# Kernel optimization log

Measured on AMD Instinct MI355X. Metric: run time of the kernel, lower is better.

## Reference

```python
import jax, jax.numpy as jnp
import numpy as np

B, L, D, H, T = 64, 512, 768, 384, 9  # batch, seq_len, hidden, hidden//2, num_tags


def setup_inputs() -> dict:
    key = jax.random.key(0)
    ks = jax.random.split(key, 8)
    return {
        "encoder_out": jax.random.normal(ks[0], (B, L, D), jnp.float32),
        "ner_labels": jax.random.randint(ks[1], (B, L), 0, T),
        "mask": jnp.ones((B, L), jnp.bool_),
        "W1": jax.random.normal(ks[2], (D, H), jnp.float32) / np.sqrt(D).astype(np.float32),
        "b1": jnp.zeros((H,), jnp.float32),
        "W2": jax.random.normal(ks[3], (H, T), jnp.float32) / np.sqrt(H).astype(np.float32),
        "b2": jnp.zeros((T,), jnp.float32),
        "start_trans": jax.random.uniform(ks[4], (T,), jnp.float32, -0.1, 0.1),
        "end_trans": jax.random.uniform(ks[5], (T,), jnp.float32, -0.1, 0.1),
        "trans": jax.random.uniform(ks[6], (T, T), jnp.float32, -0.1, 0.1),
    }


def _crf_nll(emissions, tags, mask, start_trans, end_trans, trans):
    """-mean log-likelihood, matching pytorch-crf forward (reduction='mean')."""
    maskf = mask.astype(emissions.dtype)
    # ---- numerator: score of the gold tag path ----
    emit = jnp.take_along_axis(emissions, tags[..., None], axis=-1)[..., 0]  # [B,L]
    emit_score = jnp.sum(emit * maskf, axis=1)
    tr = trans[tags[:, :-1], tags[:, 1:]]  # [B,L-1]
    tr_score = jnp.sum(tr * maskf[:, 1:], axis=1)
    last_idx = jnp.sum(mask.astype(jnp.int32), axis=1) - 1
    last_tags = jnp.take_along_axis(tags, last_idx[:, None], axis=1)[:, 0]
    numer = start_trans[tags[:, 0]] + emit_score + tr_score + end_trans[last_tags]
    # ---- denominator: forward algorithm (log partition) via scan ----
    alpha0 = start_trans[None, :] + emissions[:, 0]          # [B,T]
    em_rest = jnp.swapaxes(emissions[:, 1:], 0, 1)           # [L-1,B,T]
    mk_rest = jnp.swapaxes(maskf[:, 1:], 0, 1)               # [L-1,B]

    def step(alpha, xs):
        e_t, m_t = xs
        nxt = jax.nn.logsumexp(alpha[:, :, None] + trans[None, :, :] + e_t[:, None, :], axis=1)
        return jnp.where(m_t[:, None] > 0, nxt, alpha), None

    alpha, _ = jax.lax.scan(step, alpha0, (em_rest, mk_rest))
    denom = jax.nn.logsumexp(alpha + end_trans[None, :], axis=1)
    return -jnp.mean(numer - denom)


def reference(encoder_out, ner_labels, mask, W1, b1, W2, b2, start_trans, end_trans, trans):
    # proj: Linear -> GELU (exact erf, torch default) -> Dropout (identity in eval)
    h = jax.nn.gelu(encoder_out @ W1 + b1, approximate=False)
    emissions = h @ W2 + b2  # [B,L,T]
    return _crf_nll(emissions, ner_labels, mask, start_trans, end_trans, trans)
```

## Files before the change

kernel.cpp:

```cpp
#include <hip/hip_runtime.h>
#include <hip/hip_bf16.h>
#include <math.h>

#define B_ 64
#define L_ 512
#define D_ 768
#define H_ 384
#define T_ 9
#define M_ (B_ * L_)

typedef __attribute__((ext_vector_type(8))) short short8;
typedef __attribute__((ext_vector_type(4))) float f32x4;

__device__ __forceinline__ float gelu_exact(float x) {
    return 0.5f * x * (1.0f + erff(x * 0.70710678118654752440f));
}

__device__ __forceinline__ unsigned short f2bf(float f) {
    unsigned u = __float_as_uint(f);
    u += 0x7FFFu + ((u >> 16) & 1u);
    return (unsigned short)(u >> 16);
}

__device__ __forceinline__ float wredf(float v) {
#pragma unroll
    for (int m = 32; m >= 1; m >>= 1) v += __shfl_xor(v, m, 64);
    return v;
}

__global__ __launch_bounds__(256) void prep_kernel(
    const float* __restrict__ W1, const float* __restrict__ W2,
    unsigned short* __restrict__ W1F, unsigned short* __restrict__ W2F)
{
    const int g    = blockIdx.x * 4 + (threadIdx.x >> 6);
    const int lane = threadIdx.x & 63;
    const int lm   = lane & 15;
    const int q    = lane >> 4;
    if (g < 576) {
        const int nt = g / 24;
        const int kc = g - nt * 24;
        const int n  = nt * 16 + lm;
        short8 v;
#pragma unroll
        for (int j = 0; j < 8; ++j)
            v[j] = (short)f2bf(W1[(size_t)(kc * 32 + q * 8 + j) * H_ + n]);
        *(short8*)(W1F + ((size_t)g * 64 + lane) * 8) = v;
    } else if (g < 588) {
        const int kk = g - 576;
        short8 v;
#pragma unroll
        for (int j = 0; j < 8; ++j) {
            int k = kk * 32 + q * 8 + j;
            v[j] = (lm < 9) ? (short)f2bf(W2[(size_t)k * T_ + lm]) : (short)0;
        }
        *(short8*)(W2F + ((size_t)kk * 64 + lane) * 8) = v;
    }
}

__global__ __launch_bounds__(256, 2) void emis_mfma_kernel(
    const float* __restrict__ X,
    const unsigned short* __restrict__ W1F,
    const float* __restrict__ b1,
    const unsigned short* __restrict__ W2F,
    const float* __restrict__ b2,
    float* __restrict__ em)
{
    __shared__ unsigned short Hs[64 * 392];
    unsigned short* As = Hs;

    const int t    = threadIdx.x;
    const int lane = t & 63;
    const int w    = t >> 6;
    const int lm   = lane & 15;
    const int q    = lane >> 4;
    const int row0 = blockIdx.x * 64;

    const int ar  = t >> 2;
    const int ako = (t & 3) << 3;
    const float* xp = X + (size_t)(row0 + ar) * D_ + ako;

    f32x4 acc[4][6];
#pragma unroll
    for (int mt = 0; mt < 4; ++mt)
#pragma unroll
        for (int i = 0; i < 6; ++i) acc[mt][i] = (f32x4)0.f;

    float4 x0 = *(const float4*)(xp);
    float4 x1 = *(const float4*)(xp + 4);
    short8 bcur[6];
#pragma unroll
    for (int i = 0; i < 6; ++i)
        bcur[i] = *(const short8*)(W1F + (((size_t)(w * 6 + i) * 24) * 64 + lane) * 8);
    {
        short8 v;
        v[0] = (short)f2bf(x0.x); v[1] = (short)f2bf(x0.y);
        v[2] = (short)f2bf(x0.z); v[3] = (short)f2bf(x0.w);
        v[4] = (short)f2bf(x1.x); v[5] = (short)f2bf(x1.y);
        v[6] = (short)f2bf(x1.z); v[7] = (short)f2bf(x1.w);
        *(short8*)&As[ar * 40 + ako] = v;
    }

    int buf = 0;
    for (int kc = 0; kc < 24; ++kc) {
        const bool notlast = (kc < 23);
        float4 xn0, xn1;
        short8 bnxt[6];
        if (notlast) {
            xn0 = *(const float4*)(xp + (kc + 1) * 32);
            xn1 = *(const float4*)(xp + (kc + 1) * 32 + 4);
#pragma unroll
            for (int i = 0; i < 6; ++i)
                bnxt[i] = *(const short8*)(W1F +
                    (((size_t)(w * 6 + i) * 24 + kc + 1) * 64 + lane) * 8);
        }
        __syncthreads();
        short8 af[4];
#pragma unroll
        for (int mt = 0; mt < 4; ++mt)
            af[mt] = *(const short8*)&As[buf * 2560 + (mt * 16 + lm) * 40 + (q << 3)];
#pragma unroll
        for (int mt = 0; mt < 4; ++mt)
#pragma unroll
            for (int i = 0; i < 6; ++i)
                acc[mt][i] = __builtin_amdgcn_mfma_f32_16x16x32_bf16(
                    af[mt], bcur[i], acc[mt][i], 0, 0, 0);
        if (notlast) {
            short8 v;
            v[0] = (short)f2bf(xn0.x); v[1] = (short)f2bf(xn0.y);
            v[2] = (short)f2bf(xn0.z); v[3] = (short)f2bf(xn0.w);
            v[4] = (short)f2bf(xn1.x); v[5] = (short)f2bf(xn1.y);
            v[6] = (short)f2bf(xn1.z); v[7] = (short)f2bf(xn1.w);
            *(short8*)&As[(buf ^ 1) * 2560 + ar * 40 + ako] = v;
#pragma unroll
            for (int i = 0; i < 6; ++i) bcur[i] = bnxt[i];
            buf ^= 1;
        }
    }
    __syncthreads();

#pragma unroll
    for (int i = 0; i < 6; ++i) {
        const int col = w * 96 + i * 16 + lm;
        const float b1v = b1[col];
#pragma unroll
        for (int mt = 0; mt < 4; ++mt)
#pragma unroll
            for (int r = 0; r < 4; ++r) {
                float h = gelu_exact(acc[mt][i][r] + b1v);
                Hs[(mt * 16 + q * 4 + r) * 392 + col] = f2bf(h);
            }
    }
    __syncthreads();

    f32x4 e = (f32x4)0.f;
#pragma unroll
    for (int kk = 0; kk < 12; ++kk) {
        short8 ah = *(const short8*)&Hs[(w * 16 + lm) * 392 + kk * 32 + (q << 3)];
        short8 bw = *(const short8*)(W2F + ((size_t)(kk * 64 + lane)) * 8);
        e = __builtin_amdgcn_mfma_f32_16x16x32_bf16(ah, bw, e, 0, 0, 0);
    }
    if (lm < 9) {
        const float b2v = b2[lm];
#pragma unroll
        for (int r = 0; r < 4; ++r)
            em[(size_t)(row0 + w * 16 + q * 4 + r) * T_ + lm] = e[r] + b2v;
    }
}

__global__ __launch_bounds__(576) void crf_kernel(
    const float* __restrict__ em,
    const int* __restrict__ labels,
    const unsigned char* __restrict__ maskb,
    const float* __restrict__ st,
    const float* __restrict__ et,
    const float* __restrict__ tr,
    float* __restrict__ outb)
{
    const int b = blockIdx.x;
    const int t = threadIdx.x;

    __shared__ float es[64 * 73];
    __shared__ float Ms[64 * 81];
    __shared__ float trs[81];
    __shared__ float trsT[81];
    __shared__ float red[2];
    __shared__ unsigned char msh[L_];
    __shared__ int lbs[L_];

    const int mstride =
        (maskb[0] != 0 && maskb[1] == 0 && maskb[2] == 0 && maskb[3] == 0) ? 4 : 1;

    const float* eb = em + (size_t)b * L_ * T_;
    for (int i = t; i < L_ * T_; i += 576) {
        int tt = i / T_, j = i - tt * T_;
        es[(tt >> 3) * 73 + (tt & 7) * 9 + j] = eb[i];
    }
    if (t < 81) {
        float v = tr[t];
        trs[t] = v;
        int k = t / 9, j = t - k * 9;
        trsT[j * 9 + k] = v;
    }
    for (int i = t; i < L_; i += 576) {
        msh[i] = maskb[((size_t)b * L_ + i) * (size_t)mstride];
        lbs[i] = labels[b * L_ + i];
    }
    __syncthreads();

    {
        const int c  = t / 9;
        const int i0 = t - c * 9;
        float V[9];
#pragma unroll
        for (int j = 0; j < 9; ++j) V[j] = (j == i0) ? 0.f : -1e30f;

        const int sbeg = (c == 0) ? 1 : 0;
        for (int s = sbeg; s < 8; ++s) {
            int tt = c * 8 + s;
            if (msh[tt]) {
                const float* ep = &es[c * 73 + s * 9];
                float nv[9];
#pragma unroll
                for (int j = 0; j < 9; ++j) {
                    const float* trc = &trsT[j * 9];
                    float a[9];
#pragma unroll
                    for (int k = 0; k < 9; ++k) a[k] = V[k] + trc[k];
                    float mx = a[0];
#pragma unroll
                    for (int k = 1; k < 9; ++k) mx = fmaxf(mx, a[k]);
                    float sum = 0.f;
#pragma unroll
                    for (int k = 0; k < 9; ++k) sum += __expf(a[k] - mx);
                    nv[j] = ep[j] + mx + __logf(sum);
                }
#pragma unroll
                for (int j = 0; j < 9; ++j) V[j] = nv[j];
            }
        }
#pragma unroll
        for (int j = 0; j < 9; ++j) Ms[c * 81 + i0 * 9 + j] = V[j];
    }
    __syncthreads();

    const int lane = t & 63;
    const int w    = t >> 6;
    if (w == 0) {
        const int jj = lane < 9 ? lane : 8;
        float alpha = (lane < 9) ? st[jj] + es[jj] : -1e30f;
        for (int c = 0; c < 64; ++c) {
            float a[9];
#pragma unroll
            for (int i = 0; i < 9; ++i) {
                float av = __shfl(alpha, i, 64);
                a[i] = av + Ms[c * 81 + i * 9 + jj];
            }
            float mx = a[0];
#pragma unroll
            for (int i = 1; i < 9; ++i) mx = fmaxf(mx, a[i]);
            float sum = 0.f;
#pragma unroll
            for (int i = 0; i < 9; ++i) sum += __expf(a[i] - mx);
            float nv = mx + __logf(sum);
            if (lane < 9) alpha = nv;
        }
        float v = (lane < 9) ? alpha + et[jj] : -1e30f;
        float mx = v;
#pragma unroll
        for (int m = 32; m >= 1; m >>= 1) mx = fmaxf(mx, __shfl_xor(mx, m, 64));
        float s = __expf(v - mx);
        s = wredf(s);
        if (lane == 0) red[0] = mx + __logf(s);
    } else if (w == 1) {
        float emit_s = 0.f, tr_sc = 0.f, mcnt = 0.f;
        for (int tt = lane; tt < L_; tt += 64) {
            if (msh[tt]) {
                mcnt += 1.f;
                int tag = lbs[tt];
                emit_s += es[(tt >> 3) * 73 + (tt & 7) * 9 + tag];
                if (tt >= 1) tr_sc += trs[lbs[tt - 1] * 9 + tag];
            }
        }
        emit_s = wredf(emit_s);
        tr_sc  = wredf(tr_sc);
        mcnt   = wredf(mcnt);
        if (lane == 0) {
            int last = (int)mcnt - 1;
            red[1] = st[lbs[0]] + emit_s + tr_sc + et[lbs[last]];
        }
    }
    __syncthreads();
    if (t == 0) outb[b] = red[1] - red[0];
}

__global__ __launch_bounds__(64) void finalize_kernel(
    const float* __restrict__ bv, float* __restrict__ out)
{
    float v = bv[threadIdx.x];
    v = wredf(v);
    if (threadIdx.x == 0) out[0] = -v * (1.0f / (float)B_);
}

extern "C" void kernel_launch(void* const* d_in, const int* in_sizes, int n_in,
                              void* d_out, int out_size, void* d_ws, size_t ws_size,
                              hipStream_t stream) {
    const float*         enc    = (const float*)d_in[0];
    const int*           labels = (const int*)d_in[1];
    const unsigned char* mask   = (const unsigned char*)d_in[2];
    const float*         W1     = (const float*)d_in[3];
    const float*         b1     = (const float*)d_in[4];
    const float*         W2     = (const float*)d_in[5];
    const float*         b2     = (const float*)d_in[6];
    const float*         st     = (const float*)d_in[7];
    const float*         et     = (const float*)d_in[8];
    const float*         tr     = (const float*)d_in[9];

    float* em           = (float*)d_ws;
    float* bvals        = em + (size_t)M_ * T_;
    unsigned short* W1F = (unsigned short*)(bvals + B_);
    unsigned short* W2F = W1F + (size_t)576 * 64 * 8;

    prep_kernel<<<147, 256, 0, stream>>>(W1, W2, W1F, W2F);
    emis_mfma_kernel<<<M_ / 64, 256, 0, stream>>>(enc, W1F, b1, W2F, b2, em);
    crf_kernel<<<B_, 576, 0, stream>>>(em, labels, mask, st, et, tr, bvals);
    finalize_kernel<<<1, 64, 0, stream>>>(bvals, (float*)d_out);
}
```

Baseline: 237.3 us.

## Deepen GEMM prefetch, halve CRF chunks, fold finalize into atomic add

The emission GEMM loop is fully unrolled with a two-stage register prefetch of both X and W1 fragments, and uses a lightweight barrier (waitcnt lgkmcnt plus s_barrier) in place of __syncthreads so outstanding global loads need not drain. The CRF kernel now uses 32 chunks of 16 steps with 288 threads, caching the transition matrix in registers. The finalize kernel is removed: the output is zeroed in the prep kernel and each CRF block atomically adds its share. This trades a longer serial chunk scan and more register pressure for fewer launches and better latency hiding, and the atomic sum makes the result order nondeterministic.

```diff
diff --git a/kernel.cpp b/kernel.cpp
--- a/kernel.cpp
+++ b/kernel.cpp
@@ -28,10 +28,16 @@
     return v;
 }
 
+__device__ __forceinline__ void sync_lds() {
+    asm volatile("s_waitcnt lgkmcnt(0)\n\ts_barrier" ::: "memory");
+}
+
 __global__ __launch_bounds__(256) void prep_kernel(
     const float* __restrict__ W1, const float* __restrict__ W2,
-    unsigned short* __restrict__ W1F, unsigned short* __restrict__ W2F)
+    unsigned short* __restrict__ W1F, unsigned short* __restrict__ W2F,
+    float* __restrict__ out)
 {
+    if (blockIdx.x == 0 && threadIdx.x == 0) out[0] = 0.f;
     const int g    = blockIdx.x * 4 + (threadIdx.x >> 6);
     const int lane = threadIdx.x & 63;
     const int lm   = lane & 15;
@@ -85,55 +91,58 @@
 #pragma unroll
         for (int i = 0; i < 6; ++i) acc[mt][i] = (f32x4)0.f;
 
-    float4 x0 = *(const float4*)(xp);
-    float4 x1 = *(const float4*)(xp + 4);
-    short8 bcur[6];
-#pragma unroll
-    for (int i = 0; i < 6; ++i)
-        bcur[i] = *(const short8*)(W1F + (((size_t)(w * 6 + i) * 24) * 64 + lane) * 8);
     {
+        float4 p0 = *(const float4*)(xp);
+        float4 p1 = *(const float4*)(xp + 4);
         short8 v;
-        v[0] = (short)f2bf(x0.x); v[1] = (short)f2bf(x0.y);
-        v[2] = (short)f2bf(x0.z); v[3] = (short)f2bf(x0.w);
-        v[4] = (short)f2bf(x1.x); v[5] = (short)f2bf(x1.y);
-        v[6] = (short)f2bf(x1.z); v[7] = (short)f2bf(x1.w);
+        v[0] = (short)f2bf(p0.x); v[1] = (short)f2bf(p0.y);
+        v[2] = (short)f2bf(p0.z); v[3] = (short)f2bf(p0.w);
+        v[4] = (short)f2bf(p1.x); v[5] = (short)f2bf(p1.y);
+        v[6] = (short)f2bf(p1.z); v[7] = (short)f2bf(p1.w);
         *(short8*)&As[ar * 40 + ako] = v;
     }
-
-    int buf = 0;
+    float4 xv[2][2];
+    xv[0][0] = *(const float4*)(xp + 32);  xv[0][1] = *(const float4*)(xp + 36);
+    xv[1][0] = *(const float4*)(xp + 64);  xv[1][1] = *(const float4*)(xp + 68);
+    short8 bb[2][6];
+#pragma unroll
+    for (int i = 0; i < 6; ++i) {
+        bb[0][i] = *(const short8*)(W1F + (((size_t)(w * 6 + i) * 24 + 0) * 64 + lane) * 8);
+        bb[1][i] = *(const short8*)(W1F + (((size_t)(w * 6 + i) * 24 + 1) * 64 + lane) * 8);
+    }
+
+#pragma unroll
     for (int kc = 0; kc < 24; ++kc) {
-        const bool notlast = (kc < 23);
-        float4 xn0, xn1;
-        short8 bnxt[6];
-        if (notlast) {
-            xn0 = *(const float4*)(xp + (kc + 1) * 32);
-            xn1 = *(const float4*)(xp + (kc + 1) * 32 + 4);
-#pragma unroll
-            for (int i = 0; i < 6; ++i)
-                bnxt[i] = *(const short8*)(W1F +
-                    (((size_t)(w * 6 + i) * 24 + kc + 1) * 64 + lane) * 8);
-        }
-        __syncthreads();
+        const int s = kc & 1;
+        sync_lds();
         short8 af[4];
 #pragma unroll
         for (int mt = 0; mt < 4; ++mt)
-            af[mt] = *(const short8*)&As[buf * 2560 + (mt * 16 + lm) * 40 + (q << 3)];
+            af[mt] = *(const short8*)&As[s * 2560 + (mt * 16 + lm) * 40 + (q << 3)];
 #pragma unroll
         for (int mt = 0; mt < 4; ++mt)
 #pragma unroll
             for (int i = 0; i < 6; ++i)
                 acc[mt][i] = __builtin_amdgcn_mfma_f32_16x16x32_bf16(
-                    af[mt], bcur[i], acc[mt][i], 0, 0, 0);
-        if (notlast) {
+                    af[mt], bb[s][i], acc[mt][i], 0, 0, 0);
+        if (kc < 23) {
+            float4 x0 = xv[s][0], x1 = xv[s][1];
             short8 v;
-            v[0] = (short)f2bf(xn0.x); v[1] = (short)f2bf(xn0.y);
-            v[2] = (short)f2bf(xn0.z); v[3] = (short)f2bf(xn0.w);
-            v[4] = (short)f2bf(xn1.x); v[5] = (short)f2bf(xn1.y);
-            v[6] = (short)f2bf(xn1.z); v[7] = (short)f2bf(xn1.w);
-            *(short8*)&As[(buf ^ 1) * 2560 + ar * 40 + ako] = v;
-#pragma unroll
-            for (int i = 0; i < 6; ++i) bcur[i] = bnxt[i];
-            buf ^= 1;
+            v[0] = (short)f2bf(x0.x); v[1] = (short)f2bf(x0.y);
+            v[2] = (short)f2bf(x0.z); v[3] = (short)f2bf(x0.w);
+            v[4] = (short)f2bf(x1.x); v[5] = (short)f2bf(x1.y);
+            v[6] = (short)f2bf(x1.z); v[7] = (short)f2bf(x1.w);
+            *(short8*)&As[(s ^ 1) * 2560 + ar * 40 + ako] = v;
+            if (kc < 21) {
+                xv[s][0] = *(const float4*)(xp + (kc + 3) * 32);
+                xv[s][1] = *(const float4*)(xp + (kc + 3) * 32 + 4);
+            }
+            if (kc < 22) {
+#pragma unroll
+                for (int i = 0; i < 6; ++i)
+                    bb[s][i] = *(const short8*)(W1F +
+                        (((size_t)(w * 6 + i) * 24 + kc + 2) * 64 + lane) * 8);
+            }
         }
     }
     __syncthreads();
@@ -167,22 +176,21 @@
     }
 }
 
-__global__ __launch_bounds__(576) void crf_kernel(
+__global__ __launch_bounds__(288) void crf_kernel(
     const float* __restrict__ em,
     const int* __restrict__ labels,
     const unsigned char* __restrict__ maskb,
     const float* __restrict__ st,
     const float* __restrict__ et,
     const float* __restrict__ tr,
-    float* __restrict__ outb)
+    float* __restrict__ out)
 {
     const int b = blockIdx.x;
     const int t = threadIdx.x;
 
-    __shared__ float es[64 * 73];
-    __shared__ float Ms[64 * 81];
+    __shared__ float es[32 * 145];
+    __shared__ float Ms[32 * 81];
     __shared__ float trs[81];
-    __shared__ float trsT[81];
     __shared__ float red[2];
     __shared__ unsigned char msh[L_];
     __shared__ int lbs[L_];
@@ -191,17 +199,12 @@
         (maskb[0] != 0 && maskb[1] == 0 && maskb[2] == 0 && maskb[3] == 0) ? 4 : 1;
 
     const float* eb = em + (size_t)b * L_ * T_;
-    for (int i = t; i < L_ * T_; i += 576) {
+    for (int i = t; i < L_ * T_; i += 288) {
         int tt = i / T_, j = i - tt * T_;
-        es[(tt >> 3) * 73 + (tt & 7) * 9 + j] = eb[i];
-    }
-    if (t < 81) {
-        float v = tr[t];
-        trs[t] = v;
-        int k = t / 9, j = t - k * 9;
-        trsT[j * 9 + k] = v;
-    }
-    for (int i = t; i < L_; i += 576) {
+        es[(tt >> 4) * 145 + (tt & 15) * 9 + j] = eb[i];
+    }
+    if (t < 81) trs[t] = tr[t];
+    for (int i = t; i < L_; i += 288) {
         msh[i] = maskb[((size_t)b * L_ + i) * (size_t)mstride];
         lbs[i] = labels[b * L_ + i];
     }
@@ -210,22 +213,24 @@
     {
         const int c  = t / 9;
         const int i0 = t - c * 9;
+        float trr[81];
+#pragma unroll
+        for (int i = 0; i < 81; ++i) trr[i] = trs[i];
         float V[9];
 #pragma unroll
         for (int j = 0; j < 9; ++j) V[j] = (j == i0) ? 0.f : -1e30f;
 
         const int sbeg = (c == 0) ? 1 : 0;
-        for (int s = sbeg; s < 8; ++s) {
-            int tt = c * 8 + s;
+        for (int s = sbeg; s < 16; ++s) {
+            int tt = c * 16 + s;
             if (msh[tt]) {
-                const float* ep = &es[c * 73 + s * 9];
+                const float* ep = &es[c * 145 + s * 9];
                 float nv[9];
 #pragma unroll
                 for (int j = 0; j < 9; ++j) {
-                    const float* trc = &trsT[j * 9];
                     float a[9];
 #pragma unroll
-                    for (int k = 0; k < 9; ++k) a[k] = V[k] + trc[k];
+                    for (int k = 0; k < 9; ++k) a[k] = V[k] + trr[k * 9 + j];
                     float mx = a[0];
 #pragma unroll
                     for (int k = 1; k < 9; ++k) mx = fmaxf(mx, a[k]);
@@ -248,7 +253,7 @@
     if (w == 0) {
         const int jj = lane < 9 ? lane : 8;
         float alpha = (lane < 9) ? st[jj] + es[jj] : -1e30f;
-        for (int c = 0; c < 64; ++c) {
+        for (int c = 0; c < 32; ++c) {
             float a[9];
 #pragma unroll
             for (int i = 0; i < 9; ++i) {
@@ -277,7 +282,7 @@
             if (msh[tt]) {
                 mcnt += 1.f;
                 int tag = lbs[tt];
-                emit_s += es[(tt >> 3) * 73 + (tt & 7) * 9 + tag];
+                emit_s += es[(tt >> 4) * 145 + (tt & 15) * 9 + tag];
                 if (tt >= 1) tr_sc += trs[lbs[tt - 1] * 9 + tag];
             }
         }
@@ -290,15 +295,7 @@
         }
     }
     __syncthreads();
-    if (t == 0) outb[b] = red[1] - red[0];
-}
-
-__global__ __launch_bounds__(64) void finalize_kernel(
-    const float* __restrict__ bv, float* __restrict__ out)
-{
-    float v = bv[threadIdx.x];
-    v = wredf(v);
-    if (threadIdx.x == 0) out[0] = -v * (1.0f / (float)B_);
+    if (t == 0) atomicAdd(out, (red[0] - red[1]) * (1.0f / (float)B_));
 }
 
 extern "C" void kernel_launch(void* const* d_in, const int* in_sizes, int n_in,
@@ -316,12 +313,10 @@
     const float*         tr     = (const float*)d_in[9];
 
     float* em           = (float*)d_ws;
-    float* bvals        = em + (size_t)M_ * T_;
-    unsigned short* W1F = (unsigned short*)(bvals + B_);
+    unsigned short* W1F = (unsigned short*)(em + (size_t)M_ * T_);
     unsigned short* W2F = W1F + (size_t)576 * 64 * 8;
 
-    prep_kernel<<<147, 256, 0, stream>>>(W1, W2, W1F, W2F);
+    prep_kernel<<<147, 256, 0, stream>>>(W1, W2, W1F, W2F, (float*)d_out);
     emis_mfma_kernel<<<M_ / 64, 256, 0, stream>>>(enc, W1F, b1, W2F, b2, em);
-    crf_kernel<<<B_, 576, 0, stream>>>(em, labels, mask, st, et, tr, bvals);
-    finalize_kernel<<<1, 64, 0, stream>>>(bvals, (float*)d_out);
-}
+    crf_kernel<<<B_, 288, 0, stream>>>(em, labels, mask, st, et, tr, (float*)d_out);
+}
```

New measurement: 241.8 us. Within noise of the previous version (+1.9%).
